# Optimization experiments

Hardware: AMD Instinct MI355X
Metric: run time of the kernel (lower is better)

The kernel has to match this reference:

```python
import jax, jax.numpy as jnp
from jax import lax
import numpy as np


def tropical_conv1d(x, w, padding, mode):
    """Tropical semiring conv1d.
    y[b,o,t] = sum_c reduce_k ( x[b,c,t+k] + w[o,c,k] )
    where reduce is min (min-plus) or max (max-plus). Zero padding like nn.Conv1d.
    x: [B, C, L], w: [O, C, K] -> y: [B, O, L + 2p - K + 1]
    """
    if padding:
        x = jnp.pad(x, ((0, 0), (0, 0), (padding, padding)))
    B, C, L = x.shape
    O, _, K = w.shape
    Lo = L - K + 1
    big = jnp.array(np.inf if mode == 'min' else -np.inf, dtype=x.dtype)
    acc0 = jnp.full((B, O, C, Lo), big, dtype=x.dtype)
    red = jnp.minimum if mode == 'min' else jnp.maximum
    wk_all = jnp.moveaxis(w, 2, 0)          # [K, O, C]
    ks = jnp.arange(K)

    def step(acc, inp):
        k, wk = inp
        xs = lax.dynamic_slice_in_dim(x, k, Lo, axis=2)      # [B, C, Lo]
        v = xs[:, None, :, :] + wk[None, :, :, None]          # [B, O, C, Lo]
        return red(acc, v), None

    acc, _ = lax.scan(step, acc0, (ks, wk_all))
    return acc.sum(axis=2)                                    # [B, O, Lo]


def avg_pool1d_2(x):
    # avg_pool1d(kernel=2, stride=2), truncating odd tail like torch
    B, C, L = x.shape
    Lh = L // 2
    return x[..., : Lh * 2].reshape(B, C, Lh, 2).mean(axis=-1)


def setup_inputs() -> dict:
    key = jax.random.key(0)
    ks = jax.random.split(key, 9)
    B, Cin, L = 64, 3, 8192
    linear_size = 32448
    s = lambda k, shape, fan: jax.random.normal(k, shape, dtype=jnp.float32) * (1.0 / np.sqrt(fan))
    return {
        'input': jax.random.normal(ks[0], (B, Cin, L), dtype=jnp.float32),
        'w1': s(ks[1], (6, Cin, 80), Cin * 80),
        'w2': s(ks[2], (16, 6, 3), 6 * 3),
        'fc1_w': s(ks[3], (120, linear_size), linear_size),
        'fc1_b': jnp.zeros((120,), jnp.float32),
        'fc2_w': s(ks[4], (84, 120), 120),
        'fc2_b': jnp.zeros((84,), jnp.float32),
        'fc3_w': s(ks[5], (10, 84), 84),
        'fc3_b': jnp.zeros((10,), jnp.float32),
    }


def reference(input, w1, w2, fc1_w, fc1_b, fc2_w, fc2_b, fc3_w, fc3_b):
    x = tropical_conv1d(input, w1, padding=2, mode='min')   # [B,6,L-75]
    x = avg_pool1d_2(x)
    x = tropical_conv1d(x, w2, padding=0, mode='max')       # [B,16,L2]
    x = avg_pool1d_2(x)
    x = x.reshape(x.shape[0], -1)                            # [B, 16*floor(L2/2)]
    x = jax.nn.relu(x @ fc1_w.T + fc1_b)
    x = jax.nn.relu(x @ fc2_w.T + fc2_b)
    return x @ fc3_w.T + fc3_b
```

## Files before the change

### kernel.cpp

```cpp
#include <hip/hip_runtime.h>

#define BB 64
#define C1 3
#define LIN 8192
#define PAD1 2
#define O1 6
#define KK1 80
#define LP1 4058

#define O2 16
#define KK2 3
#define LP2 2028

#define NFLAT 32448
#define H1 120
#define H2 84
#define NOUT 10

typedef _Float16 h2 __attribute__((ext_vector_type(2)));
typedef _Float16 f16x8 __attribute__((ext_vector_type(8)));
typedef float f32x4 __attribute__((ext_vector_type(4)));
#define BIGH ((_Float16)30000.0f)

__device__ __forceinline__ h2 bch2(float f) { return __builtin_bit_cast(h2, f); }

__global__ __launch_bounds__(256) void k_prep(const float* __restrict__ w1,
                                              float* __restrict__ whb) {
  const int idx = threadIdx.x + blockIdx.x * 256;
  if (idx >= (O1 * C1) * (KK1 / 2)) return;
  const int oc = idx / (KK1 / 2);
  const int m  = idx - oc * (KK1 / 2);
  h2 v;
  v.x = (_Float16)w1[oc * KK1 + 2 * m];
  v.y = (_Float16)w1[oc * KK1 + 2 * m + 1];
  whb[idx] = __builtin_bit_cast(float, v);
}

#define TJ1 256
#define NT1 16
#define DW1 298

__global__ __launch_bounds__(256) void k_conv1(const float* __restrict__ x,
                                               const float* __restrict__ whb,
                                               float* __restrict__ p1) {
  __shared__ float AB[C1][2 * DW1 + 2];
  const int b    = blockIdx.x >> 4;
  const int tile = blockIdx.x & 15;
  const int j0   = tile * TJ1;
  const int T0   = 2 * j0;
  const int tid  = threadIdx.x;

  for (int q = tid; q < C1 * DW1; q += 256) {
    const int c = q / DW1;
    const int d = q - c * DW1;
    const int E = T0 + 2 * d - PAD1;
    const float* xc = x + ((size_t)b * C1 + c) * LIN;
    float f0 = 0.f, f1 = 0.f, f2 = 0.f;
    if ((unsigned)E < LIN) f0 = xc[E];
    if ((unsigned)(E + 1) < LIN) f1 = xc[E + 1];
    if ((unsigned)(E + 2) < LIN) f2 = xc[E + 2];
    h2 A; A.x = (_Float16)f0; A.y = (_Float16)f1;
    h2 Bv; Bv.x = (_Float16)f1; Bv.y = (_Float16)f2;
    AB[c][2 * d]     = __builtin_bit_cast(float, A);
    AB[c][2 * d + 1] = __builtin_bit_cast(float, Bv);
  }
  __syncthreads();

  const int jj = tid;
  const int j  = j0 + jj;

  float s0 = 0.f, s1 = 0.f, s2 = 0.f, s3 = 0.f, s4 = 0.f, s5 = 0.f;

#pragma unroll
  for (int c = 0; c < C1; ++c) {
    h2 aA[O1], aB[O1];
#pragma unroll
    for (int o = 0; o < O1; ++o) {
      aA[o].x = BIGH; aA[o].y = BIGH;
      aB[o].x = BIGH; aB[o].y = BIGH;
    }
#pragma unroll 2
    for (int mc = 0; mc < 10; ++mc) {
      float4 xv0 = *(const float4*)&AB[c][2 * (jj + mc * 4)];
      float4 xv1 = *(const float4*)&AB[c][2 * (jj + mc * 4) + 4];
      h2 A0 = bch2(xv0.x), B0 = bch2(xv0.y);
      h2 A1 = bch2(xv0.z), B1 = bch2(xv0.w);
      h2 A2 = bch2(xv1.x), B2 = bch2(xv1.y);
      h2 A3 = bch2(xv1.z), B3 = bch2(xv1.w);
#pragma unroll
      for (int o = 0; o < O1; ++o) {
        float4 wq = *(const float4*)&whb[(o * C1 + c) * (KK1 / 2) + mc * 4];
        h2 w0 = bch2(wq.x), w1v = bch2(wq.y), w2v = bch2(wq.z), w3v = bch2(wq.w);
        aA[o] = __builtin_elementwise_min(aA[o], A0 + w0);
        aB[o] = __builtin_elementwise_min(aB[o], B0 + w0);
        aA[o] = __builtin_elementwise_min(aA[o], A1 + w1v);
        aB[o] = __builtin_elementwise_min(aB[o], B1 + w1v);
        aA[o] = __builtin_elementwise_min(aA[o], A2 + w2v);
        aB[o] = __builtin_elementwise_min(aB[o], B2 + w2v);
        aA[o] = __builtin_elementwise_min(aA[o], A3 + w3v);
        aB[o] = __builtin_elementwise_min(aB[o], B3 + w3v);
      }
    }
    float r[O1];
#pragma unroll
    for (int o = 0; o < O1; ++o)
      r[o] = fminf((float)aA[o].x, (float)aA[o].y) + fminf((float)aB[o].x, (float)aB[o].y);
    s0 += r[0]; s1 += r[1]; s2 += r[2]; s3 += r[3]; s4 += r[4]; s5 += r[5];
  }
  if (j < LP1) {
    float* pb = p1 + (size_t)b * O1 * LP1 + j;
    pb[0 * LP1] = 0.5f * s0;
    pb[1 * LP1] = 0.5f * s1;
    pb[2 * LP1] = 0.5f * s2;
    pb[3 * LP1] = 0.5f * s3;
    pb[4 * LP1] = 0.5f * s4;
    pb[5 * LP1] = 0.5f * s5;
  }
}

#define T2 256
#define XT2 516

__global__ __launch_bounds__(256) void k_conv2(const float* __restrict__ p1,
                                               const float* __restrict__ w2,
                                               _Float16* __restrict__ p2h) {
  __shared__ float ps[O1][XT2];
  __shared__ float w2s[O2 * O1 * KK2];
  const int b    = blockIdx.x >> 3;
  const int tile = blockIdx.x & 7;
  const int j0   = tile * T2;
  const int tid  = threadIdx.x;

  for (int idx = tid; idx < O2 * O1 * KK2; idx += 256) w2s[idx] = w2[idx];
  for (int idx = tid; idx < O1 * XT2; idx += 256) {
    int c = idx / XT2;
    int p = idx - c * XT2;
    int t = 2 * j0 + p;
    ps[c][p] = (t < LP1) ? p1[((size_t)b * O1 + c) * LP1 + t] : 0.f;
  }
  __syncthreads();

  const int j = j0 + tid;
  if (j >= LP2) return;
  const int lb = 2 * tid;
  float xv[O1][4];
#pragma unroll
  for (int c = 0; c < O1; ++c) {
    xv[c][0] = ps[c][lb];     xv[c][1] = ps[c][lb + 1];
    xv[c][2] = ps[c][lb + 2]; xv[c][3] = ps[c][lb + 3];
  }
#pragma unroll
  for (int o = 0; o < O2; ++o) {
    float s = 0.f;
#pragma unroll
    for (int c = 0; c < O1; ++c) {
      float w0  = w2s[(o * O1 + c) * KK2 + 0];
      float w1v = w2s[(o * O1 + c) * KK2 + 1];
      float w2v = w2s[(o * O1 + c) * KK2 + 2];
      float m0 = fmaxf(fmaxf(xv[c][0] + w0, xv[c][1] + w1v), xv[c][2] + w2v);
      float m1 = fmaxf(fmaxf(xv[c][1] + w0, xv[c][2] + w1v), xv[c][3] + w2v);
      s += m0 + m1;
    }
    p2h[(size_t)b * NFLAT + o * LP2 + j] = (_Float16)(0.5f * s);
  }
}

#define KC2 64
#define NKC2 507

__global__ __launch_bounds__(256) void k_fc1(const _Float16* __restrict__ p2h,
                                             const float* __restrict__ w,
                                             _Float16* __restrict__ part) {
  __shared__ _Float16 bs[64][KC2];
  const int kc  = blockIdx.x;
  const int k0  = kc * KC2;
  const int tid = threadIdx.x;

#pragma unroll
  for (int r = 0; r < 2; ++r) {
    const int task = tid + 256 * r;
    const int row  = task >> 3;
    const int c4   = task & 7;
    float4 v = *(const float4*)&p2h[(size_t)row * NFLAT + k0 + c4 * 8];
    *(float4*)&bs[row][c4 * 8] = v;
  }
  __syncthreads();

  const int lane = tid & 63;
  const int wid  = tid >> 6;
  const int m_l  = lane & 15;
  const int q    = lane >> 4;
  const int m0   = wid * 32;

  const int rowA0 = m0 + m_l;
  int rowA1 = m0 + 16 + m_l;
  if (rowA1 > H1 - 1) rowA1 = H1 - 1;
  const float* wp0 = w + (size_t)rowA0 * NFLAT + k0 + q * 8;
  const float* wp1 = w + (size_t)rowA1 * NFLAT + k0 + q * 8;

  f32x4 acc[2][4];
#pragma unroll
  for (int t = 0; t < 2; ++t)
#pragma unroll
    for (int nt = 0; nt < 4; ++nt) acc[t][nt] = (f32x4){0.f, 0.f, 0.f, 0.f};

#pragma unroll
  for (int ks = 0; ks < 2; ++ks) {
    float4 a0l = *(const float4*)(wp0 + ks * 32);
    float4 a0h = *(const float4*)(wp0 + ks * 32 + 4);
    float4 a1l = *(const float4*)(wp1 + ks * 32);
    float4 a1h = *(const float4*)(wp1 + ks * 32 + 4);
    f16x8 A0, A1;
    A0[0] = (_Float16)a0l.x; A0[1] = (_Float16)a0l.y;
    A0[2] = (_Float16)a0l.z; A0[3] = (_Float16)a0l.w;
    A0[4] = (_Float16)a0h.x; A0[5] = (_Float16)a0h.y;
    A0[6] = (_Float16)a0h.z; A0[7] = (_Float16)a0h.w;
    A1[0] = (_Float16)a1l.x; A1[1] = (_Float16)a1l.y;
    A1[2] = (_Float16)a1l.z; A1[3] = (_Float16)a1l.w;
    A1[4] = (_Float16)a1h.x; A1[5] = (_Float16)a1h.y;
    A1[6] = (_Float16)a1h.z; A1[7] = (_Float16)a1h.w;
#pragma unroll
    for (int nt = 0; nt < 4; ++nt) {
      f16x8 Bf = *(const f16x8*)&bs[nt * 16 + m_l][ks * 32 + q * 8];
      acc[0][nt] = __builtin_amdgcn_mfma_f32_16x16x32_f16(A0, Bf, acc[0][nt], 0, 0, 0);
      acc[1][nt] = __builtin_amdgcn_mfma_f32_16x16x32_f16(A1, Bf, acc[1][nt], 0, 0, 0);
    }
  }

#pragma unroll
  for (int t = 0; t < 2; ++t)
#pragma unroll
    for (int nt = 0; nt < 4; ++nt)
#pragma unroll
      for (int r = 0; r < 4; ++r) {
        const int i = m0 + t * 16 + q * 4 + r;
        if (i < H1)
          part[((size_t)kc * H1 + i) * 64 + nt * 16 + m_l] = (_Float16)acc[t][nt][r];
      }
}

__global__ __launch_bounds__(512) void k_fc1red(const _Float16* __restrict__ part,
                                                float* __restrict__ part2) {
  __shared__ float red[512];
  const int bx  = blockIdx.x;
  const int s   = bx / H1;
  const int i   = bx - s * H1;
  const int tid = threadIdx.x;
  const int b   = tid & 63;
  const int sub = tid >> 6;
  const int kc0 = s * 127;
  const int kc1 = (kc0 + 127 < NKC2) ? kc0 + 127 : NKC2;
  float acc = 0.f;
  for (int kc = kc0 + sub; kc < kc1; kc += 8)
    acc += (float)part[((size_t)kc * H1 + i) * 64 + b];
  red[tid] = acc;
  __syncthreads();
  if (tid < 64) {
    float t = 0.f;
#pragma unroll
    for (int s2 = 0; s2 < 8; ++s2) t += red[b + 64 * s2];
    part2[((size_t)s * H1 + i) * 64 + b] = t;
  }
}

__global__ __launch_bounds__(128) void k_head(const float* __restrict__ part2,
                                              const float* __restrict__ fc1_b,
                                              const float* __restrict__ fc2_w,
                                              const float* __restrict__ fc2_b,
                                              const float* __restrict__ fc3_w,
                                              const float* __restrict__ fc3_b,
                                              float* __restrict__ out) {
  __shared__ float h1s[H1];
  __shared__ float h2s[H2];
  const int b = blockIdx.x;
  const int tid = threadIdx.x;
  if (tid < H1) {
    float v = part2[((size_t)0 * H1 + tid) * 64 + b]
            + part2[((size_t)1 * H1 + tid) * 64 + b]
            + part2[((size_t)2 * H1 + tid) * 64 + b]
            + part2[((size_t)3 * H1 + tid) * 64 + b];
    h1s[tid] = fmaxf(v + fc1_b[tid], 0.f);
  }
  __syncthreads();
  if (tid < H2) {
    float s = fc2_b[tid];
#pragma unroll 4
    for (int n = 0; n < H1; ++n) s += h1s[n] * fc2_w[tid * H1 + n];
    h2s[tid] = fmaxf(s, 0.f);
  }
  __syncthreads();
  if (tid < NOUT) {
    float s = fc3_b[tid];
#pragma unroll 4
    for (int n = 0; n < H2; ++n) s += h2s[n] * fc3_w[tid * H2 + n];
    out[b * NOUT + tid] = s;
  }
}

extern "C" void kernel_launch(void* const* d_in, const int* in_sizes, int n_in,
                              void* d_out, int out_size, void* d_ws, size_t ws_size,
                              hipStream_t stream) {
  const float* x     = (const float*)d_in[0];
  const float* w1    = (const float*)d_in[1];
  const float* w2    = (const float*)d_in[2];
  const float* fc1_w = (const float*)d_in[3];
  const float* fc1_b = (const float*)d_in[4];
  const float* fc2_w = (const float*)d_in[5];
  const float* fc2_b = (const float*)d_in[6];
  const float* fc3_w = (const float*)d_in[7];
  const float* fc3_b = (const float*)d_in[8];

  float* ws = (float*)d_ws;
  float*     p1    = ws;
  _Float16*  p2h   = (_Float16*)(p1 + (size_t)BB * O1 * LP1);
  _Float16*  part  = p2h + (size_t)BB * NFLAT;
  float*     part2 = (float*)(part + (size_t)NKC2 * H1 * 64);
  float*     whb   = part2 + (size_t)4 * H1 * 64;
  float*     out   = (float*)d_out;

  hipLaunchKernelGGL(k_prep, dim3(3), dim3(256), 0, stream, w1, whb);
  hipLaunchKernelGGL(k_conv1, dim3(BB * NT1), dim3(256), 0, stream, x, whb, p1);
  hipLaunchKernelGGL(k_conv2, dim3(BB * 8), dim3(256), 0, stream, p1, w2, p2h);
  hipLaunchKernelGGL(k_fc1, dim3(NKC2), dim3(256), 0, stream, p2h, fc1_w, part);
  hipLaunchKernelGGL(k_fc1red, dim3(4 * H1), dim3(512), 0, stream, part, part2);
  hipLaunchKernelGGL(k_head, dim3(BB), dim3(128), 0, stream, part2, fc1_b, fc2_w, fc2_b,
                     fc3_w, fc3_b, out);
}
```

Measured before the change: 144.5 us.

## Fuse conv1 and conv2 into one kernel and merge fc1 reduction stages

The conv1 and conv2 kernels become one, with overlapping tiles of 127 conv2 outputs. Each tile's pooled conv1 results stay in shared memory and feed the max-plus conv2 directly, so the p1 intermediate never makes a round trip through global memory and one launch is removed. Each block recomputes one extra conv1 output at the tile halo, and conv2 now runs on only half the threads per output-channel group. Separately, the two-level fc1 partial reduction collapses into a single 1024-thread kernel that also applies the bias and ReLU, which simplifies the head kernel.

Measured after the change: 142.6 us. No clear change (-1.3%).

```diff
diff --git a/kernel.cpp b/kernel.cpp
--- a/kernel.cpp
+++ b/kernel.cpp
@@ -36,23 +36,27 @@
   whb[idx] = __builtin_bit_cast(float, v);
 }
 
-#define TJ1 256
-#define NT1 16
-#define DW1 298
-
-__global__ __launch_bounds__(256) void k_conv1(const float* __restrict__ x,
-                                               const float* __restrict__ whb,
-                                               float* __restrict__ p1) {
-  __shared__ float AB[C1][2 * DW1 + 2];
-  const int b    = blockIdx.x >> 4;
-  const int tile = blockIdx.x & 15;
-  const int j0   = tile * TJ1;
-  const int T0   = 2 * j0;
+#define TILE2 127
+#define NT12 16
+#define DW12 295
+
+__global__ __launch_bounds__(256) void k_conv12(const float* __restrict__ x,
+                                                const float* __restrict__ whb,
+                                                const float* __restrict__ w2,
+                                                _Float16* __restrict__ p2h) {
+  __shared__ float AB[C1][2 * DW12 + 2];
+  __shared__ float ps[O1][256];
+  __shared__ float w2s[O2 * O1 * KK2];
+  const int tile = blockIdx.x;
+  const int b    = blockIdx.y;
+  const int pj0  = 2 * TILE2 * tile;
+  const int T0   = 2 * pj0;
   const int tid  = threadIdx.x;
 
-  for (int q = tid; q < C1 * DW1; q += 256) {
-    const int c = q / DW1;
-    const int d = q - c * DW1;
+  for (int idx = tid; idx < O2 * O1 * KK2; idx += 256) w2s[idx] = w2[idx];
+  for (int q = tid; q < C1 * DW12; q += 256) {
+    const int c = q / DW12;
+    const int d = q - c * DW12;
     const int E = T0 + 2 * d - PAD1;
     const float* xc = x + ((size_t)b * C1 + c) * LIN;
     float f0 = 0.f, f1 = 0.f, f2 = 0.f;
@@ -67,7 +71,6 @@
   __syncthreads();
 
   const int jj = tid;
-  const int j  = j0 + jj;
 
   float s0 = 0.f, s1 = 0.f, s2 = 0.f, s3 = 0.f, s4 = 0.f, s5 = 0.f;
 
@@ -107,61 +110,40 @@
       r[o] = fminf((float)aA[o].x, (float)aA[o].y) + fminf((float)aB[o].x, (float)aB[o].y);
     s0 += r[0]; s1 += r[1]; s2 += r[2]; s3 += r[3]; s4 += r[4]; s5 += r[5];
   }
-  if (j < LP1) {
-    float* pb = p1 + (size_t)b * O1 * LP1 + j;
-    pb[0 * LP1] = 0.5f * s0;
-    pb[1 * LP1] = 0.5f * s1;
-    pb[2 * LP1] = 0.5f * s2;
-    pb[3 * LP1] = 0.5f * s3;
-    pb[4 * LP1] = 0.5f * s4;
-    pb[5 * LP1] = 0.5f * s5;
-  }
-}
-
-#define T2 256
-#define XT2 516
-
-__global__ __launch_bounds__(256) void k_conv2(const float* __restrict__ p1,
-                                               const float* __restrict__ w2,
-                                               _Float16* __restrict__ p2h) {
-  __shared__ float ps[O1][XT2];
-  __shared__ float w2s[O2 * O1 * KK2];
-  const int b    = blockIdx.x >> 3;
-  const int tile = blockIdx.x & 7;
-  const int j0   = tile * T2;
-  const int tid  = threadIdx.x;
-
-  for (int idx = tid; idx < O2 * O1 * KK2; idx += 256) w2s[idx] = w2[idx];
-  for (int idx = tid; idx < O1 * XT2; idx += 256) {
-    int c = idx / XT2;
-    int p = idx - c * XT2;
-    int t = 2 * j0 + p;
-    ps[c][p] = (t < LP1) ? p1[((size_t)b * O1 + c) * LP1 + t] : 0.f;
-  }
-  __syncthreads();
-
-  const int j = j0 + tid;
-  if (j >= LP2) return;
-  const int lb = 2 * tid;
-  float xv[O1][4];
-#pragma unroll
-  for (int c = 0; c < O1; ++c) {
-    xv[c][0] = ps[c][lb];     xv[c][1] = ps[c][lb + 1];
-    xv[c][2] = ps[c][lb + 2]; xv[c][3] = ps[c][lb + 3];
-  }
-#pragma unroll
-  for (int o = 0; o < O2; ++o) {
-    float s = 0.f;
+  ps[0][jj] = 0.5f * s0;
+  ps[1][jj] = 0.5f * s1;
+  ps[2][jj] = 0.5f * s2;
+  ps[3][jj] = 0.5f * s3;
+  ps[4][jj] = 0.5f * s4;
+  ps[5][jj] = 0.5f * s5;
+  __syncthreads();
+
+  const int j2i = tid & 127;
+  const int ot  = tid >> 7;
+  const int j2  = TILE2 * tile + j2i;
+  if (j2i < TILE2 && j2 < LP2) {
+    const int lb = 2 * j2i;
+    float xv[O1][4];
 #pragma unroll
     for (int c = 0; c < O1; ++c) {
-      float w0  = w2s[(o * O1 + c) * KK2 + 0];
-      float w1v = w2s[(o * O1 + c) * KK2 + 1];
-      float w2v = w2s[(o * O1 + c) * KK2 + 2];
-      float m0 = fmaxf(fmaxf(xv[c][0] + w0, xv[c][1] + w1v), xv[c][2] + w2v);
-      float m1 = fmaxf(fmaxf(xv[c][1] + w0, xv[c][2] + w1v), xv[c][3] + w2v);
-      s += m0 + m1;
-    }
-    p2h[(size_t)b * NFLAT + o * LP2 + j] = (_Float16)(0.5f * s);
+      xv[c][0] = ps[c][lb];     xv[c][1] = ps[c][lb + 1];
+      xv[c][2] = ps[c][lb + 2]; xv[c][3] = ps[c][lb + 3];
+    }
+#pragma unroll
+    for (int oi = 0; oi < 8; ++oi) {
+      const int o = ot * 8 + oi;
+      float s = 0.f;
+#pragma unroll
+      for (int c = 0; c < O1; ++c) {
+        float w0  = w2s[(o * O1 + c) * KK2 + 0];
+        float w1v = w2s[(o * O1 + c) * KK2 + 1];
+        float w2v = w2s[(o * O1 + c) * KK2 + 2];
+        float m0 = fmaxf(fmaxf(xv[c][0] + w0, xv[c][1] + w1v), xv[c][2] + w2v);
+        float m1 = fmaxf(fmaxf(xv[c][1] + w0, xv[c][2] + w1v), xv[c][3] + w2v);
+        s += m0 + m1;
+      }
+      p2h[(size_t)b * NFLAT + o * LP2 + j2] = (_Float16)(0.5f * s);
+    }
   }
 }
 
@@ -239,32 +221,28 @@
       }
 }
 
-__global__ __launch_bounds__(512) void k_fc1red(const _Float16* __restrict__ part,
-                                                float* __restrict__ part2) {
-  __shared__ float red[512];
-  const int bx  = blockIdx.x;
-  const int s   = bx / H1;
-  const int i   = bx - s * H1;
+__global__ __launch_bounds__(1024) void k_h1(const _Float16* __restrict__ part,
+                                             const float* __restrict__ fc1_b,
+                                             float* __restrict__ h1g) {
+  __shared__ float red[1024];
+  const int i   = blockIdx.x;
   const int tid = threadIdx.x;
   const int b   = tid & 63;
   const int sub = tid >> 6;
-  const int kc0 = s * 127;
-  const int kc1 = (kc0 + 127 < NKC2) ? kc0 + 127 : NKC2;
   float acc = 0.f;
-  for (int kc = kc0 + sub; kc < kc1; kc += 8)
+  for (int kc = sub; kc < NKC2; kc += 16)
     acc += (float)part[((size_t)kc * H1 + i) * 64 + b];
   red[tid] = acc;
   __syncthreads();
   if (tid < 64) {
     float t = 0.f;
 #pragma unroll
-    for (int s2 = 0; s2 < 8; ++s2) t += red[b + 64 * s2];
-    part2[((size_t)s * H1 + i) * 64 + b] = t;
-  }
-}
-
-__global__ __launch_bounds__(128) void k_head(const float* __restrict__ part2,
-                                              const float* __restrict__ fc1_b,
+    for (int s2 = 0; s2 < 16; ++s2) t += red[b + 64 * s2];
+    h1g[i * 64 + b] = fmaxf(t + fc1_b[i], 0.f);
+  }
+}
+
+__global__ __launch_bounds__(128) void k_head(const float* __restrict__ h1g,
                                               const float* __restrict__ fc2_w,
                                               const float* __restrict__ fc2_b,
                                               const float* __restrict__ fc3_w,
@@ -274,13 +252,7 @@
   __shared__ float h2s[H2];
   const int b = blockIdx.x;
   const int tid = threadIdx.x;
-  if (tid < H1) {
-    float v = part2[((size_t)0 * H1 + tid) * 64 + b]
-            + part2[((size_t)1 * H1 + tid) * 64 + b]
-            + part2[((size_t)2 * H1 + tid) * 64 + b]
-            + part2[((size_t)3 * H1 + tid) * 64 + b];
-    h1s[tid] = fmaxf(v + fc1_b[tid], 0.f);
-  }
+  if (tid < H1) h1s[tid] = h1g[tid * 64 + b];
   __syncthreads();
   if (tid < H2) {
     float s = fc2_b[tid];
@@ -310,19 +282,16 @@
   const float* fc3_w = (const float*)d_in[7];
   const float* fc3_b = (const float*)d_in[8];
 
-  float* ws = (float*)d_ws;
-  float*     p1    = ws;
-  _Float16*  p2h   = (_Float16*)(p1 + (size_t)BB * O1 * LP1);
-  _Float16*  part  = p2h + (size_t)BB * NFLAT;
-  float*     part2 = (float*)(part + (size_t)NKC2 * H1 * 64);
-  float*     whb   = part2 + (size_t)4 * H1 * 64;
-  float*     out   = (float*)d_out;
+  _Float16* p2h  = (_Float16*)d_ws;
+  _Float16* part = p2h + (size_t)BB * NFLAT;
+  float*    h1g  = (float*)(part + (size_t)NKC2 * H1 * 64);
+  float*    whb  = h1g + (size_t)H1 * 64;
+  float*    out  = (float*)d_out;
 
   hipLaunchKernelGGL(k_prep, dim3(3), dim3(256), 0, stream, w1, whb);
-  hipLaunchKernelGGL(k_conv1, dim3(BB * NT1), dim3(256), 0, stream, x, whb, p1);
-  hipLaunchKernelGGL(k_conv2, dim3(BB * 8), dim3(256), 0, stream, p1, w2, p2h);
+  hipLaunchKernelGGL(k_conv12, dim3(NT12, BB), dim3(256), 0, stream, x, whb, w2, p2h);
   hipLaunchKernelGGL(k_fc1, dim3(NKC2), dim3(256), 0, stream, p2h, fc1_w, part);
-  hipLaunchKernelGGL(k_fc1red, dim3(4 * H1), dim3(512), 0, stream, part, part2);
-  hipLaunchKernelGGL(k_head, dim3(BB), dim3(128), 0, stream, part2, fc1_b, fc2_w, fc2_b,
+  hipLaunchKernelGGL(k_h1, dim3(H1), dim3(1024), 0, stream, part, fc1_b, h1g);
+  hipLaunchKernelGGL(k_head, dim3(BB), dim3(128), 0, stream, h1g, fc2_w, fc2_b,
                      fc3_w, fc3_b, out);
 }
```
